# Performance work log

Measured on AMD Instinct MI355X. Metric: run time of the kernel, lower is better.

## Reference

```python
import jax, jax.numpy as jnp
import numpy as np

DN = ('NCDHW', 'OIDHW', 'NCDHW')
HEADS, DIM_HEAD = 8, 64
BN_EPS = 1e-5


def conv3d(x, w, stride=1, padding=0, groups=1):
    return jax.lax.conv_general_dilated(
        x, w, window_strides=(stride,) * 3,
        padding=[(padding, padding)] * 3,
        feature_group_count=groups, dimension_numbers=DN)


def batchnorm(x, g, b, m, v):
    sh = (1, -1, 1, 1, 1)
    return (x - m.reshape(sh)) * jax.lax.rsqrt(v.reshape(sh) + BN_EPS) * g.reshape(sh) + b.reshape(sh)


def setup_inputs() -> dict:
    key = jax.random.key(0)
    ks = jax.random.split(key, 6)
    dim, inner = 128, HEADS * DIM_HEAD
    inp = {
        'x': jax.random.normal(ks[0], (4, dim, 16, 16, 16), jnp.float32),
        'wq_dw': jax.random.normal(ks[1], (dim, 1, 3, 3, 3), jnp.float32) * 0.1,
        'bn_q_g': jnp.ones((dim,), jnp.float32),
        'bn_q_b': jnp.zeros((dim,), jnp.float32),
        'bn_q_m': jnp.zeros((dim,), jnp.float32),
        'bn_q_v': jnp.ones((dim,), jnp.float32),
        'wq_pw': jax.random.normal(ks[2], (inner, dim, 1, 1, 1), jnp.float32) * 0.05,
        'wkv_dw': jax.random.normal(ks[3], (dim, 1, 3, 3, 3), jnp.float32) * 0.1,
        'bn_kv_g': jnp.ones((dim,), jnp.float32),
        'bn_kv_b': jnp.zeros((dim,), jnp.float32),
        'bn_kv_m': jnp.zeros((dim,), jnp.float32),
        'bn_kv_v': jnp.ones((dim,), jnp.float32),
        'wkv_pw': jax.random.normal(ks[4], (2 * inner, dim, 1, 1, 1), jnp.float32) * 0.05,
        'w_out': jax.random.normal(ks[5], (dim, inner, 1, 1, 1), jnp.float32) * 0.05,
        'b_out': jnp.zeros((dim,), jnp.float32),
    }
    return inp


def reference(x, wq_dw, bn_q_g, bn_q_b, bn_q_m, bn_q_v, wq_pw,
              wkv_dw, bn_kv_g, bn_kv_b, bn_kv_m, bn_kv_v, wkv_pw,
              w_out, b_out):
    b, c, z, xx, y = x.shape
    h, d = HEADS, DIM_HEAD
    inner = h * d
    scale = d ** -0.5

    # Q projection: depthwise conv (stride 1) -> BN (eval) -> pointwise conv
    q = conv3d(x, wq_dw, stride=1, padding=1, groups=c)
    q = batchnorm(q, bn_q_g, bn_q_b, bn_q_m, bn_q_v)
    q = conv3d(q, wq_pw)                      # [b, inner, z, x, y]

    # KV projection: depthwise conv (stride 2) -> BN -> pointwise conv
    kv = conv3d(x, wkv_dw, stride=2, padding=1, groups=c)
    kv = batchnorm(kv, bn_kv_g, bn_kv_b, bn_kv_m, bn_kv_v)
    kv = conv3d(kv, wkv_pw)                   # [b, 2*inner, z/2, x/2, y/2]
    k, v = kv[:, :inner], kv[:, inner:]

    nq = z * xx * y
    nk = k.shape[2] * k.shape[3] * k.shape[4]
    # channels split as (h d): reshape to [b, h, d, n]
    q4 = q.reshape(b, h, d, nq)
    k4 = k.reshape(b, h, d, nk)
    v4 = v.reshape(b, h, d, nk)

    dots = jnp.einsum('bhdi,bhdj->bhij', q4, k4) * scale   # [b,h,nq,nk]
    attn = jax.nn.softmax(dots, axis=-1)
    out = jnp.einsum('bhij,bhdj->bhdi', attn, v4)          # [b,h,d,nq]
    out = out.reshape(b, inner, z, xx, y)

    out = conv3d(out, w_out) + b_out.reshape(1, -1, 1, 1, 1)
    return out
```

## Files before the change

### kernel.cpp

```cpp
#include <hip/hip_runtime.h>
#include <hip/hip_bf16.h>

typedef __attribute__((ext_vector_type(8))) short short8;
typedef __attribute__((ext_vector_type(4))) short short4v;
typedef __attribute__((ext_vector_type(4))) float f32x4;

#define MFMA16(a, b, c) __builtin_amdgcn_mfma_f32_16x16x32_bf16((a), (b), (c), 0, 0, 0)


__device__ __forceinline__ short f2bf(float f) {
    union { __hip_bfloat16 h; short s; } u;
    u.h = __float2bfloat16(f);
    return u.s;
}

__device__ __forceinline__ unsigned pk2(float lo, float hi) {
    unsigned a = (unsigned short)f2bf(lo);
    unsigned b = (unsigned short)f2bf(hi);
    return a | (b << 16);
}

__device__ __forceinline__ short8 pack8(const f32x4 a, const f32x4 b, float s) {
    union { short8 v; unsigned w[4]; } u;
    u.w[0] = pk2(a[0] * s, a[1] * s);
    u.w[1] = pk2(a[2] * s, a[3] * s);
    u.w[2] = pk2(b[0] * s, b[1] * s);
    u.w[3] = pk2(b[2] * s, b[3] * s);
    return u.v;
}

#define C2SCALE 0.18033688011112042f

__global__ __launch_bounds__(256) void dw_kernel(
    const float* __restrict__ x,
    const float* __restrict__ wq_dw, const float* __restrict__ qg, const float* __restrict__ qb,
    const float* __restrict__ qm, const float* __restrict__ qv,
    const float* __restrict__ wkv_dw, const float* __restrict__ kg, const float* __restrict__ kb,
    const float* __restrict__ km, const float* __restrict__ kv,
    const float* __restrict__ wq_pw, const float* __restrict__ wkv_pw, const float* __restrict__ wo,
    short* __restrict__ qd_t, short* __restrict__ kvd_t,
    short* __restrict__ wq_bf, short* __restrict__ wkv_bf, short* __restrict__ wo_bf) {
    __shared__ float xs[8][3][16][17];
    const int cg = blockIdx.x, by = blockIdx.y, b = blockIdx.z;
    const int tid = threadIdx.x;

    if (by == 24) {
        const int base = (b * 16 + cg) * 256 + tid;
        for (int i = base; i < 65536; i += 16384) {
            int o = i >> 7, cin = i & 127;
            wq_bf[((o >> 4) * 4 + (cin >> 5)) * 512 + (((cin >> 3) & 3) * 16 + (o & 15)) * 8 + (cin & 7)] = f2bf(wq_pw[i]);
        }
        for (int i = base; i < 131072; i += 16384) {
            int o = i >> 7, cin = i & 127;
            wkv_bf[((o >> 4) * 4 + (cin >> 5)) * 512 + (((cin >> 3) & 3) * 16 + (o & 15)) * 8 + (cin & 7)] = f2bf(wkv_pw[i]);
        }
        for (int i = base; i < 65536; i += 16384) {
            int co = i >> 9, cin = i & 511;
            int h = cin >> 6, d2 = cin & 63;
            int m2 = d2 >> 4, gq2 = (d2 >> 2) & 3, r2 = d2 & 3;
            int frag = ((h * 2 + (m2 >> 1)) * 8 + (co >> 4));
            wo_bf[frag * 512 + (gq2 * 16 + (co & 15)) * 8 + (m2 & 1) * 4 + r2] = f2bf(wo[i]);
        }
        return;
    }

    const int y = tid >> 4, xx = tid & 15;
    const int c0 = cg * 8;

    if (by < 16) {
        const int z = by;
        #pragma unroll 4
        for (int ch = 0; ch < 8; ++ch)
            for (int zz = 0; zz < 3; ++zz) {
                int iz = z + zz - 1;
                float val = 0.f;
                if ((unsigned)iz < 16u)
                    val = x[(((b * 128 + c0 + ch) * 16 + iz) * 16 + y) * 16 + xx];
                xs[ch][zz][y][xx] = val;
            }
        __syncthreads();
        short res[8];
        #pragma unroll
        for (int ch = 0; ch < 8; ++ch) {
            const int c = c0 + ch;
            const float* wc = wq_dw + c * 27;
            float s = 0.f;
            #pragma unroll
            for (int zz = 0; zz < 3; ++zz)
                #pragma unroll
                for (int dy = 0; dy < 3; ++dy) {
                    int iy = y + dy - 1;
                    if ((unsigned)iy < 16u) {
                        float v  = xs[ch][zz][iy][xx];
                        float vm = __shfl_up(v, 1, 16);
                        float vp = __shfl_down(v, 1, 16);
                        float w0 = wc[zz * 9 + dy * 3 + 0];
                        float w1 = wc[zz * 9 + dy * 3 + 1];
                        float w2 = wc[zz * 9 + dy * 3 + 2];
                        if (xx > 0)  s += vm * w0;
                        s += v * w1;
                        if (xx < 15) s += vp * w2;
                    }
                }
            float sc = qg[c] * rsqrtf(qv[c] + 1e-5f);
            float sh = qb[c] - qm[c] * sc;
            res[ch] = f2bf(s * sc + sh);
        }
        const int i = z * 256 + tid;
        const int ib = i >> 4;
        short8 ov;
        #pragma unroll
        for (int k = 0; k < 8; ++k) ov[k] = res[k];
        *(short8*)(qd_t + (long)b * 524288 +
                   (ib * 4 + (cg >> 2)) * 512 + ((cg & 3) * 16 + xx) * 8) = ov;
    } else {
        const int oz = by - 16;
        #pragma unroll 4
        for (int ch = 0; ch < 8; ++ch)
            for (int zz = 0; zz < 3; ++zz) {
                int iz = 2 * oz + zz - 1;
                float val = 0.f;
                if ((unsigned)iz < 16u)
                    val = x[(((b * 128 + c0 + ch) * 16 + iz) * 16 + y) * 16 + xx];
                xs[ch][zz][y][xx] = val;
            }
        __syncthreads();
        const int pos = tid & 63, cq = tid >> 6;
        const int oy = pos >> 3, ox = pos & 7;
        union { unsigned u; short s[2]; } pv;
        #pragma unroll
        for (int cc = 0; cc < 2; ++cc) {
            const int chl = cq * 2 + cc;
            const int c = c0 + chl;
            const float* wc = wkv_dw + c * 27;
            float s = 0.f;
            #pragma unroll
            for (int zz = 0; zz < 3; ++zz)
                #pragma unroll
                for (int dy = 0; dy < 3; ++dy) {
                    int iy = 2 * oy + dy - 1;
                    if ((unsigned)iy < 16u) {
                        #pragma unroll
                        for (int dx = 0; dx < 3; ++dx) {
                            int ix = 2 * ox + dx - 1;
                            if ((unsigned)ix < 16u)
                                s += xs[chl][zz][iy][ix] * wc[zz * 9 + dy * 3 + dx];
                        }
                    }
                }
            float sc = kg[c] * rsqrtf(kv[c] + 1e-5f);
            float sh = kb[c] - km[c] * sc;
            pv.s[cc] = f2bf(s * sc + sh);
        }
        const int j = oz * 64 + pos;
        const int jb = j >> 4;
        *(unsigned*)(kvd_t + (long)b * 65536 +
                     (jb * 4 + (cg >> 2)) * 512 + ((cg & 3) * 16 + (j & 15)) * 8 + cq * 2) = pv.u;
    }
}

__global__ __launch_bounds__(256) void pwkv_kernel(
    const short* __restrict__ wkv_bf, const short* __restrict__ kvd_t,
    short* __restrict__ k_t, short* __restrict__ v_t) {
    const int e = blockIdx.x, b = blockIdx.y;
    const int bj16 = e >> 3, bo = e & 7;
    const int tid = threadIdx.x, lane = tid & 63, wv = tid >> 6;
    const int jl = lane & 15, gq = lane >> 4;

    short8 A[2][4];
    #pragma unroll
    for (int m = 0; m < 2; ++m) {
        const int ot = bo * 8 + wv * 2 + m;
        #pragma unroll
        for (int ks = 0; ks < 4; ++ks)
            A[m][ks] = *(const short8*)(wkv_bf + ((ot * 4 + ks) * 512) + lane * 8);
    }
    short8 Bf[4];
    #pragma unroll
    for (int ks = 0; ks < 4; ++ks)
        Bf[ks] = *(const short8*)(kvd_t + (long)b * 65536 + ((bj16 * 4 + ks) * 512) + lane * 8);

    f32x4 acc[2];
    acc[0] = (f32x4){0.f, 0.f, 0.f, 0.f};
    acc[1] = (f32x4){0.f, 0.f, 0.f, 0.f};
    #pragma unroll
    for (int ks = 0; ks < 4; ++ks) {
        acc[0] = MFMA16(A[0][ks], Bf[ks], acc[0]);
        acc[1] = MFMA16(A[1][ks], Bf[ks], acc[1]);
    }

    #pragma unroll
    for (int m = 0; m < 2; ++m) {
        const int ot = bo * 8 + wv * 2 + m;
        if (ot < 32) {
            const int h = ot >> 2, m2 = ot & 3;
            short* kf = k_t + ((long)(b * 8 + h)) * 32768;
            short4v pk;
            #pragma unroll
            for (int r = 0; r < 4; ++r) pk[r] = f2bf(acc[m][r]);
            *(short4v*)(kf + (bj16 * 2 + (m2 >> 1)) * 512 + lane * 8 + (m2 & 1) * 4) = pk;
        } else {
            const int ot2 = ot - 32;
            const int h = ot2 >> 2, md = ot2 & 3;
            short* vf = v_t + ((long)(b * 8 + h)) * 32768;
            const int frag = (bj16 >> 1) * 4 + md;
            #pragma unroll
            for (int r = 0; r < 4; ++r)
                vf[frag * 512 + ((jl >> 2) * 16 + gq * 4 + r) * 8 + (bj16 & 1) * 4 + (jl & 3)]
                    = f2bf(acc[m][r]);
        }
    }
}

__global__ __launch_bounds__(256) void fused_kernel(
    const short* __restrict__ wq_bf, const short* __restrict__ qd_t,
    const short* __restrict__ k_t, const short* __restrict__ v_t,
    const short* __restrict__ wo_bf, const float* __restrict__ bias,
    float* __restrict__ out) {
    __shared__ f32x4 lred[4][8][64];
    const int it = blockIdx.x, b = blockIdx.y;
    const int tid = threadIdx.x, lane = tid & 63, wv = tid >> 6;
    const int jl = lane & 15, gq = lane >> 4;

    short8 qdB[4];
    {
        const short* qdb = qd_t + (long)b * 524288;
        #pragma unroll
        for (int kc = 0; kc < 4; ++kc)
            qdB[kc] = *(const short8*)(qdb + (it * 4 + kc) * 512 + lane * 8);
    }

    f32x4 outacc[8];
    #pragma unroll
    for (int o = 0; o < 8; ++o) outacc[o] = (f32x4){0.f, 0.f, 0.f, 0.f};

    #pragma unroll 1
    for (int hi = 0; hi < 2; ++hi) {
        const int h = wv + hi * 4;
        const short* kf = k_t + ((long)(b * 8 + h)) * 32768;
        const short* vf = v_t + ((long)(b * 8 + h)) * 32768;
        f32x4 qa[4];
        #pragma unroll
        for (int ot = 0; ot < 4; ++ot) qa[ot] = (f32x4){0.f, 0.f, 0.f, 0.f};
        #pragma unroll
        for (int kc = 0; kc < 4; ++kc)
            #pragma unroll
            for (int ot = 0; ot < 4; ++ot) {
                short8 Af = *(const short8*)(wq_bf + (((h * 4 + ot) * 4 + kc) * 512) + lane * 8);
                qa[ot] = MFMA16(Af, qdB[kc], qa[ot]);
            }
        short8 QB[2];
        QB[0] = pack8(qa[0], qa[1], C2SCALE);
        QB[1] = pack8(qa[2], qa[3], C2SCALE);

        f32x4 O[4];
        #pragma unroll
        for (int m = 0; m < 4; ++m) O[m] = (f32x4){0.f, 0.f, 0.f, 0.f};
        float l = 0.f;

        #pragma unroll 2
        for (int c = 0; c < 8; ++c) {
            f32x4 S[4];
            #pragma unroll
            for (int n = 0; n < 4; ++n) S[n] = (f32x4){0.f, 0.f, 0.f, 0.f};
            #pragma unroll
            for (int n = 0; n < 4; ++n)
                #pragma unroll
                for (int ks = 0; ks < 2; ++ks) {
                    short8 Kf = *(const short8*)(kf + ((c * 4 + n) * 2 + ks) * 512 + lane * 8);
                    S[n] = MFMA16(Kf, QB[ks], S[n]);
                }
            short8 VA[2][4];
            #pragma unroll
            for (int ks2 = 0; ks2 < 2; ++ks2)
                #pragma unroll
                for (int m = 0; m < 4; ++m)
                    VA[ks2][m] = *(const short8*)(vf + ((c * 2 + ks2) * 4 + m) * 512 + lane * 8);
            f32x4 p[4];
            #pragma unroll
            for (int n = 0; n < 4; ++n)
                #pragma unroll
                for (int r = 0; r < 4; ++r) {
                    p[n][r] = exp2f(S[n][r]);
                    l += p[n][r];
                }
            short8 PW[2];
            PW[0] = pack8(p[0], p[1], 1.f);
            PW[1] = pack8(p[2], p[3], 1.f);
            #pragma unroll
            for (int ks2 = 0; ks2 < 2; ++ks2)
                #pragma unroll
                for (int m = 0; m < 4; ++m)
                    O[m] = MFMA16(VA[ks2][m], PW[ks2], O[m]);
        }
        l += __shfl_xor(l, 16, 64);
        l += __shfl_xor(l, 32, 64);
        float inv = 1.f / l;
        short8 PB[2];
        PB[0] = pack8(O[0], O[1], inv);
        PB[1] = pack8(O[2], O[3], inv);
        #pragma unroll
        for (int ks3 = 0; ks3 < 2; ++ks3)
            #pragma unroll
            for (int ot2 = 0; ot2 < 8; ++ot2) {
                short8 Wf = *(const short8*)(wo_bf + (((h * 2 + ks3) * 8 + ot2) * 512) + lane * 8);
                outacc[ot2] = MFMA16(Wf, PB[ks3], outacc[ot2]);
            }
    }
    #pragma unroll
    for (int ot2 = 0; ot2 < 8; ++ot2) lred[wv][ot2][lane] = outacc[ot2];
    __syncthreads();
    const int ii = it * 16 + jl;
    #pragma unroll
    for (int k2 = 0; k2 < 2; ++k2) {
        int ot2 = wv * 2 + k2;
        f32x4 s0 = lred[0][ot2][lane];
        f32x4 s1 = lred[1][ot2][lane];
        f32x4 s2 = lred[2][ot2][lane];
        f32x4 s3 = lred[3][ot2][lane];
        #pragma unroll
        for (int r = 0; r < 4; ++r) {
            int co = ot2 * 16 + gq * 4 + r;
            out[((long)(b * 128 + co)) * 4096 + ii] = s0[r] + s1[r] + s2[r] + s3[r] + bias[co];
        }
    }
}

extern "C" void kernel_launch(void* const* d_in, const int* in_sizes, int n_in,
                              void* d_out, int out_size, void* d_ws, size_t ws_size,
                              hipStream_t stream) {
    const float* x      = (const float*)d_in[0];
    const float* wq_dw  = (const float*)d_in[1];
    const float* bnq_g  = (const float*)d_in[2];
    const float* bnq_b  = (const float*)d_in[3];
    const float* bnq_m  = (const float*)d_in[4];
    const float* bnq_v  = (const float*)d_in[5];
    const float* wq_pw  = (const float*)d_in[6];
    const float* wkv_dw = (const float*)d_in[7];
    const float* bnk_g  = (const float*)d_in[8];
    const float* bnk_b  = (const float*)d_in[9];
    const float* bnk_m  = (const float*)d_in[10];
    const float* bnk_v  = (const float*)d_in[11];
    const float* wkv_pw = (const float*)d_in[12];
    const float* w_out  = (const float*)d_in[13];
    const float* b_out  = (const float*)d_in[14];
    float* out = (float*)d_out;

    char* ws = (char*)d_ws;
    short* wq_bf  = (short*)(ws + 0);
    short* wkv_bf = (short*)(ws + 131072);
    short* wo_bf  = (short*)(ws + 393216);
    short* qd_t   = (short*)(ws + 524288);
    short* kvd_t  = (short*)(ws + 4718592);
    short* k_t    = (short*)(ws + 5242880);
    short* v_t    = (short*)(ws + 7340032);

    dw_kernel<<<dim3(16, 25, 4), dim3(256), 0, stream>>>(
        x, wq_dw, bnq_g, bnq_b, bnq_m, bnq_v,
        wkv_dw, bnk_g, bnk_b, bnk_m, bnk_v,
        wq_pw, wkv_pw, w_out,
        qd_t, kvd_t, wq_bf, wkv_bf, wo_bf);
    pwkv_kernel<<<dim3(256, 4), dim3(256), 0, stream>>>(wkv_bf, kvd_t, k_t, v_t);
    fused_kernel<<<dim3(256, 4), dim3(256), 0, stream>>>(wq_bf, qd_t, k_t, v_t, wo_bf, b_out, out);
}
```

Measured before the change: 170.9 us.

## Double-buffer K fragments in attention loop and remap blocks across batches

The attention chunk loop is rewritten so K fragments for the next chunk are prefetched into registers (ping-pong KA/KB) while the current chunk computes, with setprio raised around MFMA bursts. The grid is flattened to 1D with a block-to-(batch, tile) remap that interleaves batches, presumably to spread K/V traffic across XCDs and caches. Holding an extra K buffer in registers raises register pressure and may reduce occupancy.

```diff
diff --git a/kernel.cpp b/kernel.cpp
--- a/kernel.cpp
+++ b/kernel.cpp
@@ -212,13 +212,55 @@
     }
 }
 
+#define CHUNK_BODY(cc, KCUR, KNEXT, PF)                                              \
+    {                                                                                \
+        short8 VA[8];                                                                \
+        _Pragma("unroll")                                                            \
+        for (int f = 0; f < 8; ++f)                                                  \
+            VA[f] = *(const short8*)(vf + ((cc) * 8 + f) * 512 + lane * 8);          \
+        if (PF) {                                                                    \
+            _Pragma("unroll")                                                        \
+            for (int f = 0; f < 8; ++f)                                              \
+                KNEXT[f] = *(const short8*)(kf + (((cc) + 1) * 8 + f) * 512 + lane * 8); \
+        }                                                                            \
+        f32x4 S[4];                                                                  \
+        _Pragma("unroll")                                                            \
+        for (int n = 0; n < 4; ++n) S[n] = (f32x4){0.f, 0.f, 0.f, 0.f};              \
+        __builtin_amdgcn_s_setprio(1);                                               \
+        _Pragma("unroll")                                                            \
+        for (int n = 0; n < 4; ++n) {                                                \
+            S[n] = MFMA16(KCUR[n * 2 + 0], QB[0], S[n]);                             \
+            S[n] = MFMA16(KCUR[n * 2 + 1], QB[1], S[n]);                             \
+        }                                                                            \
+        __builtin_amdgcn_s_setprio(0);                                               \
+        _Pragma("unroll")                                                            \
+        for (int n = 0; n < 4; ++n)                                                  \
+            _Pragma("unroll")                                                        \
+            for (int r = 0; r < 4; ++r) {                                            \
+                S[n][r] = exp2f(S[n][r]);                                            \
+                l += S[n][r];                                                        \
+            }                                                                        \
+        short8 PW[2];                                                                \
+        PW[0] = pack8(S[0], S[1], 1.f);                                              \
+        PW[1] = pack8(S[2], S[3], 1.f);                                              \
+        __builtin_amdgcn_s_setprio(1);                                               \
+        _Pragma("unroll")                                                            \
+        for (int m = 0; m < 4; ++m) {                                                \
+            O[m] = MFMA16(VA[m], PW[0], O[m]);                                       \
+            O[m] = MFMA16(VA[4 + m], PW[1], O[m]);                                   \
+        }                                                                            \
+        __builtin_amdgcn_s_setprio(0);                                               \
+    }
+
 __global__ __launch_bounds__(256) void fused_kernel(
     const short* __restrict__ wq_bf, const short* __restrict__ qd_t,
     const short* __restrict__ k_t, const short* __restrict__ v_t,
     const short* __restrict__ wo_bf, const float* __restrict__ bias,
     float* __restrict__ out) {
     __shared__ f32x4 lred[4][8][64];
-    const int it = blockIdx.x, b = blockIdx.y;
+    const int bid = blockIdx.x;
+    const int b = (bid & 7) >> 1;
+    const int it = ((bid >> 3) << 1) | (bid & 1);
     const int tid = threadIdx.x, lane = tid & 63, wv = tid >> 6;
     const int jl = lane & 15, gq = lane >> 4;
 
@@ -258,41 +300,18 @@
         for (int m = 0; m < 4; ++m) O[m] = (f32x4){0.f, 0.f, 0.f, 0.f};
         float l = 0.f;
 
-        #pragma unroll 2
-        for (int c = 0; c < 8; ++c) {
-            f32x4 S[4];
-            #pragma unroll
-            for (int n = 0; n < 4; ++n) S[n] = (f32x4){0.f, 0.f, 0.f, 0.f};
-            #pragma unroll
-            for (int n = 0; n < 4; ++n)
-                #pragma unroll
-                for (int ks = 0; ks < 2; ++ks) {
-                    short8 Kf = *(const short8*)(kf + ((c * 4 + n) * 2 + ks) * 512 + lane * 8);
-                    S[n] = MFMA16(Kf, QB[ks], S[n]);
-                }
-            short8 VA[2][4];
-            #pragma unroll
-            for (int ks2 = 0; ks2 < 2; ++ks2)
-                #pragma unroll
-                for (int m = 0; m < 4; ++m)
-                    VA[ks2][m] = *(const short8*)(vf + ((c * 2 + ks2) * 4 + m) * 512 + lane * 8);
-            f32x4 p[4];
-            #pragma unroll
-            for (int n = 0; n < 4; ++n)
-                #pragma unroll
-                for (int r = 0; r < 4; ++r) {
-                    p[n][r] = exp2f(S[n][r]);
-                    l += p[n][r];
-                }
-            short8 PW[2];
-            PW[0] = pack8(p[0], p[1], 1.f);
-            PW[1] = pack8(p[2], p[3], 1.f);
-            #pragma unroll
-            for (int ks2 = 0; ks2 < 2; ++ks2)
-                #pragma unroll
-                for (int m = 0; m < 4; ++m)
-                    O[m] = MFMA16(VA[ks2][m], PW[ks2], O[m]);
-        }
+        short8 KA[8], KB[8];
+        #pragma unroll
+        for (int f = 0; f < 8; ++f)
+            KA[f] = *(const short8*)(kf + f * 512 + lane * 8);
+
+        #pragma unroll 1
+        for (int cp = 0; cp < 4; ++cp) {
+            const int c0c = cp * 2;
+            CHUNK_BODY(c0c, KA, KB, 1)
+            CHUNK_BODY(c0c + 1, KB, KA, (cp < 3))
+        }
+
         l += __shfl_xor(l, 16, 64);
         l += __shfl_xor(l, 32, 64);
         float inv = 1.f / l;
@@ -361,5 +380,5 @@
         wq_pw, wkv_pw, w_out,
         qd_t, kvd_t, wq_bf, wkv_bf, wo_bf);
     pwkv_kernel<<<dim3(256, 4), dim3(256), 0, stream>>>(wkv_bf, kvd_t, k_t, v_t);
-    fused_kernel<<<dim3(256, 4), dim3(256), 0, stream>>>(wq_bf, qd_t, k_t, v_t, wo_bf, b_out, out);
-}
+    fused_kernel<<<dim3(1024), dim3(256), 0, stream>>>(wq_bf, qd_t, k_t, v_t, wo_bf, b_out, out);
+}
```

Measured after the change: 162.2 us. 1.05x faster.
